# Optimization experiments

Measured on AMD Instinct MI355X. Metric: run time of the kernel, lower is better.

## Reference

```python
import jax, jax.numpy as jnp
import numpy as np

BITS = 4
GROUPSIZE = 128
IN_FEATURES = 4096
OUT_FEATURES = 11008
N_GROUPS = IN_FEATURES // GROUPSIZE  # 32
MASK = (1 << BITS) - 1  # 15


def setup_inputs() -> dict:
    key = jax.random.key(0)
    ks = jax.random.split(key, 5)
    x = jax.random.normal(ks[0], (2, 2048, IN_FEATURES), dtype=jnp.float32)
    qweight = jax.random.randint(ks[1], (IN_FEATURES // 8, OUT_FEATURES), 0, 2**31 - 1, dtype=jnp.int32)
    qzeros = jax.random.randint(ks[2], (N_GROUPS, OUT_FEATURES // 8), 0, 2**31 - 1, dtype=jnp.int32)
    scales = jax.random.uniform(ks[3], (N_GROUPS, OUT_FEATURES), dtype=jnp.float16)
    bias = jax.random.normal(ks[4], (OUT_FEATURES,), dtype=jnp.float32)
    return {"x": x, "qweight": qweight, "qzeros": qzeros, "scales": scales, "bias": bias}


def _dequant(qweight, qzeros, scales):
    # wf = [0, 4, 8, ..., 28]: bit offsets of the 8 int4 nibbles in each int32
    wf = jnp.arange(0, 32, BITS, dtype=jnp.int32)
    # unpack weights: [IN//8, OUT] -> [IN//8, 8, OUT] -> [N_GROUPS, GROUPSIZE, OUT]
    w = (qweight[:, None, :] >> wf[None, :, None]) & MASK
    w = w.reshape(N_GROUPS, GROUPSIZE, OUT_FEATURES).astype(jnp.float32)
    # unpack zeros: [NG, OUT//8] -> [NG, OUT//8, 8] -> [NG, 1, OUT]
    z = (qzeros[:, :, None] >> wf[None, None, :]) & MASK
    z = z.reshape(N_GROUPS, 1, OUT_FEATURES).astype(jnp.float32)
    s = scales.astype(jnp.float32)[:, None, :]  # [NG, 1, OUT]
    # scales * w - scales * z, per group; fused elementwise
    return (s * (w - z)).reshape(IN_FEATURES, OUT_FEATURES)


def reference(x, qweight, qzeros, scales, bias):
    W = _dequant(qweight, qzeros, scales)  # [IN, OUT] fp32
    out = jnp.matmul(x.astype(jnp.float32), W) + bias
    return out
```

## Files before the change

### kernel.cpp

```cpp
#include <hip/hip_runtime.h>
#include <hip/hip_fp16.h>

#define K_DIM 4096
#define N_DIM 11008
#define NZ8   1376
#define BM    256
#define BN    256
#define BK    64
#define NT_N  43
#define NKT   64
#define ATB   32768

typedef _Float16 f16x8 __attribute__((ext_vector_type(8)));
typedef float    f32x4 __attribute__((ext_vector_type(4)));

__device__ __forceinline__ f16x8 dq8(unsigned q, __half2 scp, __half2 nzp)
{
    const unsigned mu = 0xE400E400u;
    const __half2 m1024 = *(const __half2*)&mu;
    union { __half2 h2[4]; f16x8 v; } p;
#pragma unroll
    for (int d = 0; d < 4; ++d) {
        unsigned t = ((q >> (4 * d)) & 0x000F000Fu) | 0x64006400u;
        p.h2[d] = __hfma2(__hadd2(*(const __half2*)&t, m1024), scp, nzp);
    }
    return p.v;
}

__global__ __launch_bounds__(256)
void r11_xcvt(const float* __restrict__ x, __half* __restrict__ xh, int nchunks)
{
    int c = blockIdx.x * 256 + threadIdx.x;
    const int stride = gridDim.x * 256;
    for (; c < nchunks; c += stride) {
        const int w    = c & 2047;
        const int tidx = c >> 11;
        const int row  = w >> 3;
        const int s    = w & 7;
        const int ls   = s ^ (row & 7);
        const int mt   = tidx >> 6;
        const int kt   = tidx & 63;
        const size_t gm = (size_t)mt * 256 + row;
        const int kb   = kt * 64 + ls * 8;
        const float4 f0 = *(const float4*)(x + gm * K_DIM + kb);
        const float4 f1 = *(const float4*)(x + gm * K_DIM + kb + 4);
        union { __half2 h2[4]; int4 v; } p;
        p.h2[0] = __floats2half2_rn(f0.x, f1.x);
        p.h2[1] = __floats2half2_rn(f0.y, f1.y);
        p.h2[2] = __floats2half2_rn(f0.z, f1.z);
        p.h2[3] = __floats2half2_rn(f0.w, f1.w);
        ((int4*)xh)[c] = p.v;
    }
}

__device__ __forceinline__ void stage_a_cvt(const float* __restrict__ x,
                                            unsigned char* __restrict__ abuf,
                                            int bm0, int kt, int arow, int ahalf, int asw)
{
    const float* src = x + (size_t)(bm0 + arow) * K_DIM + kt * 64 + ahalf * 32;
    unsigned char* aw = abuf + arow * 128;
#pragma unroll
    for (int c = 0; c < 4; ++c) {
        const float4 f0 = *(const float4*)(src + c * 8);
        const float4 f1 = *(const float4*)(src + c * 8 + 4);
        union { __half2 h2[4]; f16x8 v; } p;
        p.h2[0] = __floats2half2_rn(f0.x, f1.x);
        p.h2[1] = __floats2half2_rn(f0.y, f1.y);
        p.h2[2] = __floats2half2_rn(f0.z, f1.z);
        p.h2[3] = __floats2half2_rn(f0.w, f1.w);
        *(f16x8*)(aw + ((((ahalf * 4 + c) << 4) ^ asw))) = p.v;
    }
}

template<int APATH>
__global__ __launch_bounds__(512, 2)
void r11_gemm(const float* __restrict__ x,
              const __half* __restrict__ xh,
              const int*   __restrict__ qweight,
              const int*   __restrict__ qzeros,
              const float* __restrict__ scales,
              const float* __restrict__ bias,
              float* __restrict__ out)
{
    __shared__ __align__(16) unsigned char Asm[2][ATB];
    __shared__ __align__(16) unsigned char Bsm[2][ATB];

    const int tid  = threadIdx.x;
    const int lane = tid & 63;
    const int wid  = tid >> 6;
    const int wr   = (wid >> 2) * 128;
    const int wc   = (wid & 3) * 64;

    int bid = blockIdx.x;
    const int cpx = gridDim.x >> 3;
    bid = (bid & 7) * cpx + (bid >> 3);
    const int bm0 = (bid / NT_N) * BM;
    const int bn0 = (bid % NT_N) * BN;

    const int bnn = tid & 255;
    const int bq  = tid >> 8;
    const int ngl = bn0 + bnn;
    const int* qwp = qweight + (size_t)bq * N_DIM + ngl;
    const int bsw = bnn & 7;

    const char* agp = (const char*)xh + ((size_t)(bm0 >> 8) * NKT) * ATB + tid * 16;

    const int arow = tid >> 1, ahalf = tid & 1;
    const int asw  = (arow & 7) << 4;

    const int frow = lane & 15, kb8 = lane >> 4, fsw = frow & 7;

    f32x4 acc[8][4];
#pragma unroll
    for (int m = 0; m < 8; ++m)
#pragma unroll
        for (int n = 0; n < 4; ++n)
            acc[m][n] = (f32x4){0.f, 0.f, 0.f, 0.f};

    __half2 scp, nzp;
    {
        const float sc = scales[ngl];
        const unsigned zq = (unsigned)qzeros[ngl >> 3];
        const float zf = (float)((zq >> ((ngl & 7) * 4)) & 15u);
        const __half sh = __float2half_rn(sc), nh = __float2half_rn(-sc * zf);
        scp = __half2(sh, sh); nzp = __half2(nh, nh);
    }

    if constexpr (APATH == 0) {
#pragma unroll
        for (int i = 0; i < 4; ++i)
            __builtin_amdgcn_global_load_lds((const unsigned int*)(agp + i * 8192),
                                             (unsigned int*)&Asm[0][tid * 16 + i * 8192],
                                             16, 0, 0);
    } else {
        stage_a_cvt(x, &Asm[0][0], bm0, 0, arow, ahalf, asw);
    }
    {
        unsigned q[4];
#pragma unroll
        for (int i = 0; i < 4; ++i) q[i] = (unsigned)qwp[(size_t)(2 * i) * N_DIM];
#pragma unroll
        for (int i = 0; i < 4; ++i)
            *(f16x8*)(&Bsm[0][bnn * 128 + (((bq + 2 * i) ^ bsw) << 4)]) = dq8(q[i], scp, nzp);
    }
    __syncthreads();

    for (int kt = 0; kt < NKT; ++kt) {
        const int cur = kt & 1, nxt = cur ^ 1;
        unsigned qn[4];
        const bool hn = (kt + 1 < NKT);

        if (hn) {
            if constexpr (APATH == 0) {
                const char* ag = agp + (size_t)(kt + 1) * ATB;
#pragma unroll
                for (int i = 0; i < 4; ++i)
                    __builtin_amdgcn_global_load_lds((const unsigned int*)(ag + i * 8192),
                                                     (unsigned int*)&Asm[nxt][tid * 16 + i * 8192],
                                                     16, 0, 0);
            }
#pragma unroll
            for (int i = 0; i < 4; ++i)
                qn[i] = (unsigned)qwp[(size_t)((kt + 1) * 8 + 2 * i) * N_DIM];
            if (((kt + 1) & 1) == 0) {
                const int g = (kt + 1) >> 1;
                const float sc = scales[(size_t)g * N_DIM + ngl];
                const unsigned zq = (unsigned)qzeros[(size_t)g * NZ8 + (ngl >> 3)];
                const float zf = (float)((zq >> ((ngl & 7) * 4)) & 15u);
                const __half sh = __float2half_rn(sc), nh = __float2half_rn(-sc * zf);
                scp = __half2(sh, sh); nzp = __half2(nh, nh);
            }
        }

#pragma unroll
        for (int kh = 0; kh < 2; ++kh) {
            const int ksl = (kh << 2) + kb8;
            f16x8 bfr[4];
#pragma unroll
            for (int n = 0; n < 4; ++n) {
                const int nn = wc + n * 16 + frow;
                bfr[n] = *(const f16x8*)(&Bsm[cur][nn * 128 + (((ksl ^ fsw) << 4))]);
            }
#pragma unroll
            for (int m = 0; m < 8; ++m) {
                const int row = wr + m * 16 + frow;
                const f16x8 af = *(const f16x8*)(&Asm[cur][row * 128 + (((ksl ^ fsw) << 4))]);
#pragma unroll
                for (int n = 0; n < 4; ++n)
                    acc[m][n] = __builtin_amdgcn_mfma_f32_16x16x32_f16(
                        af, bfr[n], acc[m][n], 0, 0, 0);
            }
        }

        if (hn) {
            if constexpr (APATH == 1)
                stage_a_cvt(x, &Asm[nxt][0], bm0, kt + 1, arow, ahalf, asw);
#pragma unroll
            for (int i = 0; i < 4; ++i)
                *(f16x8*)(&Bsm[nxt][bnn * 128 + (((bq + 2 * i) ^ bsw) << 4)]) = dq8(qn[i], scp, nzp);
        }
        __syncthreads();
    }

    const int crow0 = (lane >> 4) << 2, ccol = lane & 15;
#pragma unroll
    for (int n = 0; n < 4; ++n) {
        const int col = bn0 + wc + n * 16 + ccol;
        const float bv = bias[col];
#pragma unroll
        for (int m = 0; m < 8; ++m) {
            const int row = bm0 + wr + m * 16 + crow0;
#pragma unroll
            for (int j = 0; j < 4; ++j)
                out[(size_t)(row + j) * N_DIM + col] = acc[m][n][j] + bv;
        }
    }
}

extern "C" void kernel_launch(void* const* d_in, const int* in_sizes, int n_in,
                              void* d_out, int out_size, void* d_ws, size_t ws_size,
                              hipStream_t stream)
{
    const float* x   = (const float*)d_in[0];
    const int*   qw  = (const int*)d_in[1];
    const int*   qz  = (const int*)d_in[2];
    const float* scl = (const float*)d_in[3];
    const float* bs  = (const float*)d_in[4];
    float* out = (float*)d_out;

    const int M = in_sizes[0] / K_DIM;
    const size_t xh_bytes = (size_t)M * K_DIM * 2;
    dim3 grid((M / BM) * NT_N);

    if (ws_size >= xh_bytes) {
        __half* xh = (__half*)d_ws;
        const int nchunks = M * K_DIM / 8;
        hipLaunchKernelGGL(r11_xcvt, dim3(2048), dim3(256), 0, stream, x, xh, nchunks);
        hipLaunchKernelGGL((r11_gemm<0>), grid, dim3(512), 0, stream,
                           x, xh, qw, qz, scl, bs, out);
    } else {
        hipLaunchKernelGGL((r11_gemm<1>), grid, dim3(512), 0, stream,
                           x, (const __half*)nullptr, qw, qz, scl, bs, out);
    }
}
```

Measured before the change: 407.2 us.

## Restructure GEMM main loop into barrier-phased LDS loads and prioritized MFMA clusters

Splits each K-tile into four phases. Each phase loads A/B fragments from LDS, synchronizes the workgroup, then issues a 16-MFMA cluster under raised wave priority (s_setprio). Global prefetch of weights and scales is issued early, and dequant/store of the next B tile is moved between phases so it overlaps with MFMA work from other waves. The intent is ping-pong style interleaving of memory and matrix ops across waves. The cost is several extra s_barriers per tile and explicit lgkmcnt/vmcnt waits that may serialize work.

```diff
diff --git a/kernel.cpp b/kernel.cpp
--- a/kernel.cpp
+++ b/kernel.cpp
@@ -14,6 +14,12 @@
 typedef _Float16 f16x8 __attribute__((ext_vector_type(8)));
 typedef float    f32x4 __attribute__((ext_vector_type(4)));
 
+#define LGKM0() do { asm volatile("s_waitcnt lgkmcnt(0)" ::: "memory"); \
+                     __builtin_amdgcn_sched_barrier(0); } while (0)
+#define VMC0()  do { asm volatile("s_waitcnt vmcnt(0)"   ::: "memory"); \
+                     __builtin_amdgcn_sched_barrier(0); } while (0)
+#define BAR()   __builtin_amdgcn_s_barrier()
+
 __device__ __forceinline__ f16x8 dq8(unsigned q, __half2 scp, __half2 nzp)
 {
     const unsigned mu = 0xE400E400u;
@@ -28,7 +34,7 @@
 }
 
 __global__ __launch_bounds__(256)
-void r11_xcvt(const float* __restrict__ x, __half* __restrict__ xh, int nchunks)
+void r12_xcvt(const float* __restrict__ x, __half* __restrict__ xh, int nchunks)
 {
     int c = blockIdx.x * 256 + threadIdx.x;
     const int stride = gridDim.x * 256;
@@ -74,7 +80,7 @@
 
 template<int APATH>
 __global__ __launch_bounds__(512, 2)
-void r11_gemm(const float* __restrict__ x,
+void r12_gemm(const float* __restrict__ x,
               const __half* __restrict__ xh,
               const int*   __restrict__ qweight,
               const int*   __restrict__ qzeros,
@@ -100,15 +106,18 @@
     const int bnn = tid & 255;
     const int bq  = tid >> 8;
     const int ngl = bn0 + bnn;
-    const int* qwp = qweight + (size_t)bq * N_DIM + ngl;
+    const int* qwp = qwp = qweight + (size_t)bq * N_DIM + ngl;
     const int bsw = bnn & 7;
 
     const char* agp = (const char*)xh + ((size_t)(bm0 >> 8) * NKT) * ATB + tid * 16;
-
     const int arow = tid >> 1, ahalf = tid & 1;
     const int asw  = (arow & 7) << 4;
 
     const int frow = lane & 15, kb8 = lane >> 4, fsw = frow & 7;
+    const int aBase = (wr + frow) * 128;
+    const int bBase = (wc + frow) * 128;
+    const int so0 = ((kb8 ^ fsw) << 4);
+    const int so1 = (((4 + kb8) ^ fsw) << 4);
 
     f32x4 acc[8][4];
 #pragma unroll
@@ -145,11 +154,25 @@
     }
     __syncthreads();
 
+    float    nsc = 0.f;
+    unsigned nzq = 0u;
+
     for (int kt = 0; kt < NKT; ++kt) {
         const int cur = kt & 1, nxt = cur ^ 1;
-        unsigned qn[4];
         const bool hn = (kt + 1 < NKT);
-
+        unsigned qn0 = 0, qn1 = 0, qn2 = 0, qn3 = 0;
+        const unsigned char* Ac = &Asm[cur][0];
+        const unsigned char* Bc = &Bsm[cur][0];
+        f16x8 a0, a1, a2, a3, b0, b1, b2, b3;
+
+        a0 = *(const f16x8*)(Ac + aBase + 0 * 2048 + so0);
+        a1 = *(const f16x8*)(Ac + aBase + 1 * 2048 + so0);
+        a2 = *(const f16x8*)(Ac + aBase + 2 * 2048 + so0);
+        a3 = *(const f16x8*)(Ac + aBase + 3 * 2048 + so0);
+        b0 = *(const f16x8*)(Bc + bBase + 0 * 2048 + so0);
+        b1 = *(const f16x8*)(Bc + bBase + 1 * 2048 + so0);
+        b2 = *(const f16x8*)(Bc + bBase + 2 * 2048 + so0);
+        b3 = *(const f16x8*)(Bc + bBase + 3 * 2048 + so0);
         if (hn) {
             if constexpr (APATH == 0) {
                 const char* ag = agp + (size_t)(kt + 1) * ATB;
@@ -159,46 +182,97 @@
                                                      (unsigned int*)&Asm[nxt][tid * 16 + i * 8192],
                                                      16, 0, 0);
             }
-#pragma unroll
-            for (int i = 0; i < 4; ++i)
-                qn[i] = (unsigned)qwp[(size_t)((kt + 1) * 8 + 2 * i) * N_DIM];
+            qn0 = (unsigned)qwp[(size_t)((kt + 1) * 8 + 0) * N_DIM];
+            qn1 = (unsigned)qwp[(size_t)((kt + 1) * 8 + 2) * N_DIM];
+            qn2 = (unsigned)qwp[(size_t)((kt + 1) * 8 + 4) * N_DIM];
+            qn3 = (unsigned)qwp[(size_t)((kt + 1) * 8 + 6) * N_DIM];
             if (((kt + 1) & 1) == 0) {
                 const int g = (kt + 1) >> 1;
-                const float sc = scales[(size_t)g * N_DIM + ngl];
-                const unsigned zq = (unsigned)qzeros[(size_t)g * NZ8 + (ngl >> 3)];
-                const float zf = (float)((zq >> ((ngl & 7) * 4)) & 15u);
-                const __half sh = __float2half_rn(sc), nh = __float2half_rn(-sc * zf);
+                nsc = scales[(size_t)g * N_DIM + ngl];
+                nzq = (unsigned)qzeros[(size_t)g * NZ8 + (ngl >> 3)];
+            }
+        }
+        BAR(); LGKM0();
+        __builtin_amdgcn_s_setprio(1);
+#pragma unroll
+        for (int n = 0; n < 4; ++n) {
+            const f16x8 bb = (n == 0) ? b0 : (n == 1) ? b1 : (n == 2) ? b2 : b3;
+            acc[0][n] = __builtin_amdgcn_mfma_f32_16x16x32_f16(a0, bb, acc[0][n], 0, 0, 0);
+            acc[1][n] = __builtin_amdgcn_mfma_f32_16x16x32_f16(a1, bb, acc[1][n], 0, 0, 0);
+            acc[2][n] = __builtin_amdgcn_mfma_f32_16x16x32_f16(a2, bb, acc[2][n], 0, 0, 0);
+            acc[3][n] = __builtin_amdgcn_mfma_f32_16x16x32_f16(a3, bb, acc[3][n], 0, 0, 0);
+        }
+        __builtin_amdgcn_s_setprio(0);
+        BAR();
+
+        a0 = *(const f16x8*)(Ac + aBase + 8192 + 0 * 2048 + so0);
+        a1 = *(const f16x8*)(Ac + aBase + 8192 + 1 * 2048 + so0);
+        a2 = *(const f16x8*)(Ac + aBase + 8192 + 2 * 2048 + so0);
+        a3 = *(const f16x8*)(Ac + aBase + 8192 + 3 * 2048 + so0);
+        BAR(); LGKM0();
+        __builtin_amdgcn_s_setprio(1);
+#pragma unroll
+        for (int n = 0; n < 4; ++n) {
+            const f16x8 bb = (n == 0) ? b0 : (n == 1) ? b1 : (n == 2) ? b2 : b3;
+            acc[4][n] = __builtin_amdgcn_mfma_f32_16x16x32_f16(a0, bb, acc[4][n], 0, 0, 0);
+            acc[5][n] = __builtin_amdgcn_mfma_f32_16x16x32_f16(a1, bb, acc[5][n], 0, 0, 0);
+            acc[6][n] = __builtin_amdgcn_mfma_f32_16x16x32_f16(a2, bb, acc[6][n], 0, 0, 0);
+            acc[7][n] = __builtin_amdgcn_mfma_f32_16x16x32_f16(a3, bb, acc[7][n], 0, 0, 0);
+        }
+        __builtin_amdgcn_s_setprio(0);
+        BAR();
+
+        a0 = *(const f16x8*)(Ac + aBase + 0 * 2048 + so1);
+        a1 = *(const f16x8*)(Ac + aBase + 1 * 2048 + so1);
+        a2 = *(const f16x8*)(Ac + aBase + 2 * 2048 + so1);
+        a3 = *(const f16x8*)(Ac + aBase + 3 * 2048 + so1);
+        b0 = *(const f16x8*)(Bc + bBase + 0 * 2048 + so1);
+        b1 = *(const f16x8*)(Bc + bBase + 1 * 2048 + so1);
+        b2 = *(const f16x8*)(Bc + bBase + 2 * 2048 + so1);
+        b3 = *(const f16x8*)(Bc + bBase + 3 * 2048 + so1);
+        BAR(); LGKM0();
+        __builtin_amdgcn_s_setprio(1);
+#pragma unroll
+        for (int n = 0; n < 4; ++n) {
+            const f16x8 bb = (n == 0) ? b0 : (n == 1) ? b1 : (n == 2) ? b2 : b3;
+            acc[0][n] = __builtin_amdgcn_mfma_f32_16x16x32_f16(a0, bb, acc[0][n], 0, 0, 0);
+            acc[1][n] = __builtin_amdgcn_mfma_f32_16x16x32_f16(a1, bb, acc[1][n], 0, 0, 0);
+            acc[2][n] = __builtin_amdgcn_mfma_f32_16x16x32_f16(a2, bb, acc[2][n], 0, 0, 0);
+            acc[3][n] = __builtin_amdgcn_mfma_f32_16x16x32_f16(a3, bb, acc[3][n], 0, 0, 0);
+        }
+        __builtin_amdgcn_s_setprio(0);
+        BAR();
+
+        a0 = *(const f16x8*)(Ac + aBase + 8192 + 0 * 2048 + so1);
+        a1 = *(const f16x8*)(Ac + aBase + 8192 + 1 * 2048 + so1);
+        a2 = *(const f16x8*)(Ac + aBase + 8192 + 2 * 2048 + so1);
+        a3 = *(const f16x8*)(Ac + aBase + 8192 + 3 * 2048 + so1);
+        if (hn) {
+            if (((kt + 1) & 1) == 0) {
+                const float zf = (float)((nzq >> ((ngl & 7) * 4)) & 15u);
+                const __half sh = __float2half_rn(nsc), nh = __float2half_rn(-nsc * zf);
                 scp = __half2(sh, sh); nzp = __half2(nh, nh);
             }
-        }
-
-#pragma unroll
-        for (int kh = 0; kh < 2; ++kh) {
-            const int ksl = (kh << 2) + kb8;
-            f16x8 bfr[4];
-#pragma unroll
-            for (int n = 0; n < 4; ++n) {
-                const int nn = wc + n * 16 + frow;
-                bfr[n] = *(const f16x8*)(&Bsm[cur][nn * 128 + (((ksl ^ fsw) << 4))]);
-            }
-#pragma unroll
-            for (int m = 0; m < 8; ++m) {
-                const int row = wr + m * 16 + frow;
-                const f16x8 af = *(const f16x8*)(&Asm[cur][row * 128 + (((ksl ^ fsw) << 4))]);
-#pragma unroll
-                for (int n = 0; n < 4; ++n)
-                    acc[m][n] = __builtin_amdgcn_mfma_f32_16x16x32_f16(
-                        af, bfr[n], acc[m][n], 0, 0, 0);
-            }
-        }
-
-        if (hn) {
+            unsigned char* bw = &Bsm[nxt][bnn * 128];
+            *(f16x8*)(bw + (((bq + 0) ^ bsw) << 4)) = dq8(qn0, scp, nzp);
+            *(f16x8*)(bw + (((bq + 2) ^ bsw) << 4)) = dq8(qn1, scp, nzp);
+            *(f16x8*)(bw + (((bq + 4) ^ bsw) << 4)) = dq8(qn2, scp, nzp);
+            *(f16x8*)(bw + (((bq + 6) ^ bsw) << 4)) = dq8(qn3, scp, nzp);
             if constexpr (APATH == 1)
                 stage_a_cvt(x, &Asm[nxt][0], bm0, kt + 1, arow, ahalf, asw);
-#pragma unroll
-            for (int i = 0; i < 4; ++i)
-                *(f16x8*)(&Bsm[nxt][bnn * 128 + (((bq + 2 * i) ^ bsw) << 4)]) = dq8(qn[i], scp, nzp);
-        }
+        }
+        BAR(); LGKM0();
+        __builtin_amdgcn_s_setprio(1);
+#pragma unroll
+        for (int n = 0; n < 4; ++n) {
+            const f16x8 bb = (n == 0) ? b0 : (n == 1) ? b1 : (n == 2) ? b2 : b3;
+            acc[4][n] = __builtin_amdgcn_mfma_f32_16x16x32_f16(a0, bb, acc[4][n], 0, 0, 0);
+            acc[5][n] = __builtin_amdgcn_mfma_f32_16x16x32_f16(a1, bb, acc[5][n], 0, 0, 0);
+            acc[6][n] = __builtin_amdgcn_mfma_f32_16x16x32_f16(a2, bb, acc[6][n], 0, 0, 0);
+            acc[7][n] = __builtin_amdgcn_mfma_f32_16x16x32_f16(a3, bb, acc[7][n], 0, 0, 0);
+        }
+        __builtin_amdgcn_s_setprio(0);
+        VMC0();
         __syncthreads();
     }
 
@@ -235,11 +309,11 @@
     if (ws_size >= xh_bytes) {
         __half* xh = (__half*)d_ws;
         const int nchunks = M * K_DIM / 8;
-        hipLaunchKernelGGL(r11_xcvt, dim3(2048), dim3(256), 0, stream, x, xh, nchunks);
-        hipLaunchKernelGGL((r11_gemm<0>), grid, dim3(512), 0, stream,
+        hipLaunchKernelGGL(r12_xcvt, dim3(2048), dim3(256), 0, stream, x, xh, nchunks);
+        hipLaunchKernelGGL((r12_gemm<0>), grid, dim3(512), 0, stream,
                            x, xh, qw, qz, scl, bs, out);
     } else {
-        hipLaunchKernelGGL((r11_gemm<1>), grid, dim3(512), 0, stream,
+        hipLaunchKernelGGL((r12_gemm<1>), grid, dim3(512), 0, stream,
                            x, (const __half*)nullptr, qw, qz, scl, bs, out);
     }
 }
```

Measured after the change: 422.0 us. 1.04x slower.
